# Performance work log

Hardware: AMD Instinct MI355X
Metric: run time of the kernel (lower is better)

## Reference

```python
import jax, jax.numpy as jnp
import numpy as np

TOP_K = 2


def setup_inputs() -> dict:
    key = jax.random.key(0)
    ks = jax.random.split(key, 5)
    B, S, H, E, F = 4, 1024, 1024, 16, 4096
    scale = 0.02
    return {
        "input_tensor": jax.random.normal(ks[0], (B, S, H), dtype=jnp.float32),
        "Wg": scale * jax.random.normal(ks[1], (H, E), dtype=jnp.float32),
        "bg": jnp.zeros((E,), dtype=jnp.float32),
        "W1": scale * jax.random.normal(ks[2], (E, H, F), dtype=jnp.float32),
        "b1": jnp.zeros((E, F), dtype=jnp.float32),
        "W2": scale * jax.random.normal(ks[3], (E, F, H), dtype=jnp.float32),
        "b2": jnp.zeros((E, H), dtype=jnp.float32),
    }


def reference(input_tensor, Wg, bg, W1, b1, W2, b2):
    # Faithful to DualOutputMoE.forward_first_pass: the per-(b,s,k) Python loop
    # plus _weighted_sum collapses ALL token expert outputs into a single
    # [1,1,H] vector normalized by the total routing weight (= B*S).
    B, S, H = input_tensor.shape
    T = B * S
    E = Wg.shape[1]
    x = input_tensor.reshape(T, H)

    routing_scores = x @ Wg + bg                    # [T, E] (raw gate logits)
    top_v, top_i = jax.lax.top_k(routing_scores, TOP_K)
    top_w = jax.nn.softmax(top_v, axis=-1)          # per-token top-k weights

    # combine[t, e] = sum_k top_w[t, k] * 1[top_i[t, k] == e]
    combine = jnp.zeros((T, E), x.dtype).at[jnp.arange(T)[:, None], top_i].add(top_w)
    total_weight = top_w.sum()                      # matches python sum of .item()s

    def expert_step(acc, params):
        w1, bb1, w2, bb2, c = params                # c: [T] combine weights for this expert
        y = jax.nn.gelu(x @ w1 + bb1, approximate=False) @ w2 + bb2  # [T, H]
        return acc + c @ y, None

    acc0 = jnp.zeros((H,), x.dtype)
    acc, _ = jax.lax.scan(expert_step, acc0, (W1, b1, W2, b2, combine.T))
    first_output = (acc / total_weight).reshape(1, 1, H)
    return first_output
```

## Files before the change

### kernel.cpp

```cpp
#include <hip/hip_runtime.h>
#include <hip/hip_bf16.h>
#include <math.h>

typedef __bf16 bf16_t;
typedef __bf16 bf16x4 __attribute__((ext_vector_type(4)));
typedef __bf16 bf16x8 __attribute__((ext_vector_type(8)));
typedef float  f32x4  __attribute__((ext_vector_type(4)));

#define T_TOK 4096
#define H_DIM 1024
#define E_NUM 16
#define F_DIM 4096
#define CH_ROWS 128
#define CH_MAX  32

#define WS_E0     0
#define WS_E1     16384
#define WS_W0     32768
#define WS_W1     49152
#define WS_COUNTS 65536
#define WS_SUMW   65664
#define WS_XOFF   65792
#define WS_LIDX   131072
#define WS_LW     393216
#define WS_GPART  655360
#define WS_P2     655360
#define WS_G      9043968
#define WS_XE     9306112

#define AS_GLOBAL(p) ((const __attribute__((address_space(1))) void*)(p))
#define AS_LDS(p)    ((__attribute__((address_space(3))) void*)(p))

__global__ __launch_bounds__(64) void k_route(const float* __restrict__ x,
    const float* __restrict__ Wg, const float* __restrict__ bg,
    int* __restrict__ e0, int* __restrict__ e1,
    float* __restrict__ w0, float* __restrict__ w1)
{
    const int t = blockIdx.x;
    const int lane = threadIdx.x;
    const float* xr = x + (size_t)t * H_DIM;

    float s[E_NUM];
#pragma unroll
    for (int e = 0; e < E_NUM; ++e) s[e] = 0.f;

#pragma unroll
    for (int i = 0; i < 16; ++i) {
        const int h = i * 64 + lane;
        const float xv = xr[h];
        const float4* wr = (const float4*)(Wg + (size_t)h * E_NUM);
        float4 q0 = wr[0], q1 = wr[1], q2 = wr[2], q3 = wr[3];
        s[0] += xv*q0.x;  s[1] += xv*q0.y;  s[2] += xv*q0.z;  s[3] += xv*q0.w;
        s[4] += xv*q1.x;  s[5] += xv*q1.y;  s[6] += xv*q1.z;  s[7] += xv*q1.w;
        s[8] += xv*q2.x;  s[9] += xv*q2.y;  s[10]+= xv*q2.z;  s[11]+= xv*q2.w;
        s[12]+= xv*q3.x;  s[13]+= xv*q3.y;  s[14]+= xv*q3.z;  s[15]+= xv*q3.w;
    }
#pragma unroll
    for (int off = 32; off >= 1; off >>= 1) {
#pragma unroll
        for (int e = 0; e < E_NUM; ++e) s[e] += __shfl_xor(s[e], off);
    }
    if (lane == 0) {
#pragma unroll
        for (int e = 0; e < E_NUM; ++e) s[e] += bg[e];
        float b1v = -3e38f; int i1 = 0;
#pragma unroll
        for (int e = 0; e < E_NUM; ++e) { if (s[e] > b1v) { b1v = s[e]; i1 = e; } }
        float b2v = -3e38f; int i2 = 0;
#pragma unroll
        for (int e = 0; e < E_NUM; ++e) { if (e != i1 && s[e] > b2v) { b2v = s[e]; i2 = e; } }
        const float ex  = expf(b2v - b1v);
        const float inv = 1.f / (1.f + ex);
        e0[t] = i1; e1[t] = i2;
        w0[t] = inv; w1[t] = ex * inv;
    }
}

__global__ __launch_bounds__(64) void k_lists(const int* __restrict__ e0, const int* __restrict__ e1,
    const float* __restrict__ w0, const float* __restrict__ w1,
    int* __restrict__ lidx, float* __restrict__ lw,
    int* __restrict__ counts, float* __restrict__ sumw)
{
    const int e = blockIdx.x;
    const int lane = threadIdx.x;
    int cnt = 0; float sw = 0.f;
    for (int base = 0; base < T_TOK; base += 64) {
        const int t = base + lane;
        const bool m0 = (e0[t] == e);
        const bool m1 = (e1[t] == e);
        const bool m  = m0 | m1;
        const unsigned long long bal = __ballot(m);
        const int pos = cnt + __popcll(bal & ((1ull << lane) - 1ull));
        if (m) {
            const float w = m0 ? w0[t] : w1[t];
            lidx[e * T_TOK + pos] = t;
            lw[e * T_TOK + pos]   = w;
            sw += w;
        }
        cnt += __popcll(bal);
    }
#pragma unroll
    for (int off = 32; off >= 1; off >>= 1) sw += __shfl_xor(sw, off);
    if (lane == 0) { counts[e] = cnt; sumw[e] = sw; }
}

__global__ void k_scan(const int* __restrict__ counts, int* __restrict__ xoff) {
    if (threadIdx.x == 0) {
        int o = 0;
        for (int e = 0; e < E_NUM; ++e) { xoff[e] = o; o += (counts[e] + CH_ROWS - 1) & ~(CH_ROWS - 1); }
    }
}

__global__ __launch_bounds__(256) void k_gather(const float* __restrict__ x,
    const int* __restrict__ lidx, const int* __restrict__ counts,
    const int* __restrict__ xoff, bf16_t* __restrict__ Xe)
{
    const int chunk = blockIdx.x >> 2;
    const int part  = blockIdx.x & 3;
    const int e = blockIdx.y;
    const int cnt = counts[e];
    const int start = chunk * CH_ROWS;
    if (chunk && start >= cnt) return;
    const int tid = threadIdx.x;
    const size_t rbase = (size_t)xoff[e] + start;

    for (int it = part * 16; it < part * 16 + 16; ++it) {
        const int task = it * 256 + tid;
        const int rl   = task >> 7;
        const int sc   = task & 127;
        const int row  = start + rl;
        bf16x8 v8 = {};
        if (row < cnt) {
            const int tok = lidx[e * T_TOK + row];
            const int l   = (sc & 7) ^ (rl & 7);
            const int k   = (sc >> 3) * 64 + l * 8;
            const float4 a = *(const float4*)(x + (size_t)tok * H_DIM + k);
            const float4 b = *(const float4*)(x + (size_t)tok * H_DIM + k + 4);
            v8[0]=(bf16_t)a.x; v8[1]=(bf16_t)a.y; v8[2]=(bf16_t)a.z; v8[3]=(bf16_t)a.w;
            v8[4]=(bf16_t)b.x; v8[5]=(bf16_t)b.y; v8[6]=(bf16_t)b.z; v8[7]=(bf16_t)b.w;
        }
        *(bf16x8*)(Xe + (rbase + rl) * H_DIM + sc * 8) = v8;
    }
}

__global__ __launch_bounds__(256, 3) void k_expert(
    const float* __restrict__ W1, const float* __restrict__ b1,
    const bf16_t* __restrict__ Xe, const float* __restrict__ lw,
    const int* __restrict__ counts, const int* __restrict__ xoff,
    float* __restrict__ gpart)
{
    const int ftile = blockIdx.x;
    const int chunk = blockIdx.y;
    const int e     = blockIdx.z;
    const int cnt   = counts[e];
    const int start = chunk * CH_ROWS;
    if (chunk && start >= cnt) return;

    __shared__ __align__(16) bf16_t Alds[2][CH_ROWS * 64];
    __shared__ __align__(16) bf16_t Blds[2][64 * 72];
    __shared__ float w_s[CH_ROWS];
    __shared__ float b1_s[64];
    __shared__ float gred[2][64];

    const int tid  = threadIdx.x;
    const int lane = tid & 63;
    const int wid  = tid >> 6;
    const int wm   = wid & 1;
    const int wn   = wid >> 1;
    const int lr   = lane & 15;
    const int lg   = lane >> 4;

    if (tid < CH_ROWS) {
        const int r = start + tid;
        w_s[tid] = (r < cnt) ? lw[e * T_TOK + r] : 0.f;
    } else if (tid < CH_ROWS + 64) {
        b1_s[tid - CH_ROWS] = b1[(size_t)e * F_DIM + ftile * 64 + (tid - CH_ROWS)];
    }

    f32x4 acc[4][2];
#pragma unroll
    for (int i = 0; i < 4; ++i)
#pragma unroll
        for (int j = 0; j < 2; ++j)
#pragma unroll
            for (int q = 0; q < 4; ++q) acc[i][j][q] = 0.f;

    const bf16_t* Asrc = Xe + ((size_t)xoff[e] + start) * H_DIM;
    const float*  W1p  = W1 + (size_t)e * H_DIM * F_DIM + (size_t)ftile * 64 + lane;

    const int arow = (wid * 4) * 8 + (lane >> 3);
    const int acol = lane & 7;

    float bv[16];

    {
        const float* wp = W1p + (size_t)(wid * 16) * F_DIM;
#pragma unroll
        for (int j = 0; j < 16; ++j) bv[j] = wp[(size_t)j * F_DIM];
#pragma unroll
        for (int p = 0; p < 4; ++p) {
            const int seg = wid * 4 + p;
            const bf16_t* src = Asrc + (size_t)(seg * 8 + (lane >> 3)) * H_DIM + acol * 8;
            __builtin_amdgcn_global_load_lds(AS_GLOBAL(src),
                AS_LDS((char*)&Alds[0][0] + seg * 1024), 16, 0, 0);
        }
        bf16x8 pk0, pk1;
#pragma unroll
        for (int q = 0; q < 8; ++q) { pk0[q] = (bf16_t)bv[q]; pk1[q] = (bf16_t)bv[8 + q]; }
        bf16_t* bdst = &Blds[0][lane * 72 + wid * 16];
        *(bf16x8*)bdst       = pk0;
        *(bf16x8*)(bdst + 8) = pk1;
    }
    __syncthreads();

    int cur = 0;
    for (int t = 0; t < H_DIM / 64; ++t) {
        const int nxt = cur ^ 1;
        const bool more = (t + 1) < (H_DIM / 64);
        if (more) {
            const int k0 = (t + 1) * 64;
            const float* wp = W1p + (size_t)(k0 + wid * 16) * F_DIM;
#pragma unroll
            for (int j = 0; j < 16; ++j) bv[j] = wp[(size_t)j * F_DIM];
#pragma unroll
            for (int p = 0; p < 4; ++p) {
                const int seg = wid * 4 + p;
                const bf16_t* src = Asrc + (size_t)(seg * 8 + (lane >> 3)) * H_DIM + k0 + acol * 8;
                __builtin_amdgcn_global_load_lds(AS_GLOBAL(src),
                    AS_LDS((char*)&Alds[nxt][0] + seg * 1024), 16, 0, 0);
            }
        }
#pragma unroll
        for (int kh = 0; kh < 2; ++kh) {
            bf16x8 af[4], bfr[2];
#pragma unroll
            for (int mf = 0; mf < 4; ++mf) {
                const int r = wm * 64 + mf * 16 + lr;
                const int eoff = (kh * 32 + lg * 8) ^ ((r & 7) * 8);
                af[mf] = *(const bf16x8*)&Alds[cur][r * 64 + eoff];
            }
#pragma unroll
            for (int nf = 0; nf < 2; ++nf)
                bfr[nf] = *(const bf16x8*)&Blds[cur][(wn * 32 + nf * 16 + lr) * 72 + kh * 32 + lg * 8];
#pragma unroll
            for (int mf = 0; mf < 4; ++mf)
#pragma unroll
                for (int nf = 0; nf < 2; ++nf)
                    acc[mf][nf] = __builtin_amdgcn_mfma_f32_16x16x32_bf16(af[mf], bfr[nf], acc[mf][nf], 0, 0, 0);
        }
        if (more) {
            bf16x8 pk0, pk1;
#pragma unroll
            for (int q = 0; q < 8; ++q) { pk0[q] = (bf16_t)bv[q]; pk1[q] = (bf16_t)bv[8 + q]; }
            bf16_t* bdst = &Blds[nxt][lane * 72 + wid * 16];
            *(bf16x8*)bdst       = pk0;
            *(bf16x8*)(bdst + 8) = pk1;
        }
        __syncthreads();
        cur = nxt;
    }

    float gcol[2] = {0.f, 0.f};
#pragma unroll
    for (int nf = 0; nf < 2; ++nf) {
        const float bb = b1_s[wn * 32 + nf * 16 + lr];
#pragma unroll
        for (int mf = 0; mf < 4; ++mf) {
#pragma unroll
            for (int i = 0; i < 4; ++i) {
                const int row = wm * 64 + mf * 16 + lg * 4 + i;
                const float h  = acc[mf][nf][i] + bb;
                const float gl = 0.5f * h * (1.f + erff(h * 0.70710678118654752f));
                gcol[nf] += w_s[row] * gl;
            }
        }
    }
#pragma unroll
    for (int nf = 0; nf < 2; ++nf) {
        gcol[nf] += __shfl_xor(gcol[nf], 16);
        gcol[nf] += __shfl_xor(gcol[nf], 32);
    }
    if (lane < 16) {
#pragma unroll
        for (int nf = 0; nf < 2; ++nf) gred[wm][wn * 32 + nf * 16 + lane] = gcol[nf];
    }
    __syncthreads();
    if (tid < 64) {
        const float sum = gred[0][tid] + gred[1][tid];
        gpart[(size_t)(e * CH_MAX + chunk) * F_DIM + ftile * 64 + tid] = sum;
    }
}

__global__ __launch_bounds__(256) void k_redg(const float* __restrict__ gpart,
    const int* __restrict__ counts, float* __restrict__ g)
{
    const int e = blockIdx.y;
    const int f = blockIdx.x * 256 + threadIdx.x;
    const int nch = (counts[e] + CH_ROWS - 1) / CH_ROWS;
    float s = 0.f;
    for (int c = 0; c < nch; ++c)
        s += gpart[(size_t)(e * CH_MAX + c) * F_DIM + f];
    g[(size_t)e * F_DIM + f] = s;
}

__global__ __launch_bounds__(256) void k_out1(const float* __restrict__ g,
    const float* __restrict__ W2, float* __restrict__ p2)
{
    const int fc = blockIdx.x;
    const int e  = blockIdx.y;
    const int tid = threadIdx.x;
    __shared__ float gs[128];
    if (tid < 128) gs[tid] = g[(size_t)e * F_DIM + fc * 128 + tid];
    __syncthreads();
    const float* W2p = W2 + (size_t)e * F_DIM * H_DIM + (size_t)fc * 128 * H_DIM;
    float ax = 0.f, ay = 0.f, az = 0.f, aw = 0.f;
#pragma unroll 8
    for (int f = 0; f < 128; ++f) {
        const float gv = gs[f];
        const float4 wv = *(const float4*)(W2p + (size_t)f * H_DIM + tid * 4);
        ax += gv * wv.x; ay += gv * wv.y; az += gv * wv.z; aw += gv * wv.w;
    }
    float4 st; st.x = ax; st.y = ay; st.z = az; st.w = aw;
    *(float4*)(p2 + (size_t)(e * 32 + fc) * H_DIM + tid * 4) = st;
}

__global__ __launch_bounds__(256) void k_out2(const float* __restrict__ p2,
    const float* __restrict__ sumw, const float* __restrict__ b2, float* __restrict__ out)
{
    const int tid = threadIdx.x;
    const int hh  = tid & 31;
    const int seg = tid >> 5;
    const int h   = blockIdx.x * 32 + hh;
    float s = 0.f;
    for (int j = 0; j < 64; ++j)
        s += p2[(size_t)(seg * 64 + j) * H_DIM + h];
    __shared__ float red[8][33];
    red[seg][hh] = s;
    __syncthreads();
    if (tid < 32) {
        const int h2 = blockIdx.x * 32 + tid;
        float tot = 0.f;
#pragma unroll
        for (int q = 0; q < 8; ++q) tot += red[q][tid];
        float tw = 0.f, bias = 0.f;
#pragma unroll
        for (int e = 0; e < E_NUM; ++e) { tw += sumw[e]; bias += sumw[e] * b2[e * H_DIM + h2]; }
        out[h2] = (tot + bias) / tw;
    }
}

extern "C" void kernel_launch(void* const* d_in, const int* in_sizes, int n_in,
                              void* d_out, int out_size, void* d_ws, size_t ws_size,
                              hipStream_t stream) {
    const float* x  = (const float*)d_in[0];
    const float* Wg = (const float*)d_in[1];
    const float* bg = (const float*)d_in[2];
    const float* W1 = (const float*)d_in[3];
    const float* b1 = (const float*)d_in[4];
    const float* W2 = (const float*)d_in[5];
    const float* b2 = (const float*)d_in[6];
    float* out = (float*)d_out;

    char* ws = (char*)d_ws;
    int*    e0     = (int*)(ws + WS_E0);
    int*    e1     = (int*)(ws + WS_E1);
    float*  w0     = (float*)(ws + WS_W0);
    float*  w1     = (float*)(ws + WS_W1);
    int*    counts = (int*)(ws + WS_COUNTS);
    float*  sumw   = (float*)(ws + WS_SUMW);
    int*    xoff   = (int*)(ws + WS_XOFF);
    int*    lidx   = (int*)(ws + WS_LIDX);
    float*  lw     = (float*)(ws + WS_LW);
    float*  gpart  = (float*)(ws + WS_GPART);
    float*  g      = (float*)(ws + WS_G);
    float*  p2     = (float*)(ws + WS_P2);
    bf16_t* Xe     = (bf16_t*)(ws + WS_XE);

    k_route<<<T_TOK, 64, 0, stream>>>(x, Wg, bg, e0, e1, w0, w1);
    k_lists<<<E_NUM, 64, 0, stream>>>(e0, e1, w0, w1, lidx, lw, counts, sumw);
    k_scan<<<1, 64, 0, stream>>>(counts, xoff);
    k_gather<<<dim3(CH_MAX * 4, E_NUM), 256, 0, stream>>>(x, lidx, counts, xoff, Xe);
    k_expert<<<dim3(F_DIM / 64, CH_MAX, E_NUM), 256, 0, stream>>>(W1, b1, Xe, lw, counts, xoff, gpart);
    k_redg<<<dim3(F_DIM / 256, E_NUM), 256, 0, stream>>>(gpart, counts, g);
    k_out1<<<dim3(32, E_NUM), 256, 0, stream>>>(g, W2, p2);
    k_out2<<<32, 256, 0, stream>>>(p2, sumw, b2, out);
}
```

Baseline: 313.5 us.

## Widen expert GEMM F tile to 128 and deepen W1 prefetch pipeline

Result: no change. 308.9 us (-1.5%).

```diff
diff --git a/kernel.cpp b/kernel.cpp
--- a/kernel.cpp
+++ b/kernel.cpp
@@ -143,7 +143,7 @@
     }
 }
 
-__global__ __launch_bounds__(256, 3) void k_expert(
+__global__ __launch_bounds__(256, 2) void k_expert(
     const float* __restrict__ W1, const float* __restrict__ b1,
     const bf16_t* __restrict__ Xe, const float* __restrict__ lw,
     const int* __restrict__ counts, const int* __restrict__ xoff,
@@ -157,10 +157,10 @@
     if (chunk && start >= cnt) return;
 
     __shared__ __align__(16) bf16_t Alds[2][CH_ROWS * 64];
-    __shared__ __align__(16) bf16_t Blds[2][64 * 72];
+    __shared__ __align__(16) bf16_t Blds[2][128 * 72];
     __shared__ float w_s[CH_ROWS];
-    __shared__ float b1_s[64];
-    __shared__ float gred[2][64];
+    __shared__ float b1_s[128];
+    __shared__ float gred[2][128];
 
     const int tid  = threadIdx.x;
     const int lane = tid & 63;
@@ -173,97 +173,99 @@
     if (tid < CH_ROWS) {
         const int r = start + tid;
         w_s[tid] = (r < cnt) ? lw[e * T_TOK + r] : 0.f;
-    } else if (tid < CH_ROWS + 64) {
-        b1_s[tid - CH_ROWS] = b1[(size_t)e * F_DIM + ftile * 64 + (tid - CH_ROWS)];
-    }
-
-    f32x4 acc[4][2];
+    }
+    if (tid < 128) b1_s[tid] = b1[(size_t)e * F_DIM + ftile * 128 + tid];
+
+    f32x4 acc[4][4];
 #pragma unroll
     for (int i = 0; i < 4; ++i)
 #pragma unroll
-        for (int j = 0; j < 2; ++j)
+        for (int j = 0; j < 4; ++j)
 #pragma unroll
             for (int q = 0; q < 4; ++q) acc[i][j][q] = 0.f;
 
     const bf16_t* Asrc = Xe + ((size_t)xoff[e] + start) * H_DIM;
-    const float*  W1p  = W1 + (size_t)e * H_DIM * F_DIM + (size_t)ftile * 64 + lane;
-
-    const int arow = (wid * 4) * 8 + (lane >> 3);
-    const int acol = lane & 7;
-
-    float bv[16];
-
-    {
-        const float* wp = W1p + (size_t)(wid * 16) * F_DIM;
-#pragma unroll
-        for (int j = 0; j < 16; ++j) bv[j] = wp[(size_t)j * F_DIM];
-#pragma unroll
-        for (int p = 0; p < 4; ++p) {
-            const int seg = wid * 4 + p;
-            const bf16_t* src = Asrc + (size_t)(seg * 8 + (lane >> 3)) * H_DIM + acol * 8;
-            __builtin_amdgcn_global_load_lds(AS_GLOBAL(src),
-                AS_LDS((char*)&Alds[0][0] + seg * 1024), 16, 0, 0);
-        }
-        bf16x8 pk0, pk1;
-#pragma unroll
-        for (int q = 0; q < 8; ++q) { pk0[q] = (bf16_t)bv[q]; pk1[q] = (bf16_t)bv[8 + q]; }
-        bf16_t* bdst = &Blds[0][lane * 72 + wid * 16];
-        *(bf16x8*)bdst       = pk0;
-        *(bf16x8*)(bdst + 8) = pk1;
-    }
-    __syncthreads();
-
-    int cur = 0;
-    for (int t = 0; t < H_DIM / 64; ++t) {
-        const int nxt = cur ^ 1;
-        const bool more = (t + 1) < (H_DIM / 64);
-        if (more) {
-            const int k0 = (t + 1) * 64;
-            const float* wp = W1p + (size_t)(k0 + wid * 16) * F_DIM;
-#pragma unroll
-            for (int j = 0; j < 16; ++j) bv[j] = wp[(size_t)j * F_DIM];
-#pragma unroll
-            for (int p = 0; p < 4; ++p) {
-                const int seg = wid * 4 + p;
-                const bf16_t* src = Asrc + (size_t)(seg * 8 + (lane >> 3)) * H_DIM + k0 + acol * 8;
-                __builtin_amdgcn_global_load_lds(AS_GLOBAL(src),
-                    AS_LDS((char*)&Alds[nxt][0] + seg * 1024), 16, 0, 0);
-            }
-        }
-#pragma unroll
-        for (int kh = 0; kh < 2; ++kh) {
-            bf16x8 af[4], bfr[2];
-#pragma unroll
-            for (int mf = 0; mf < 4; ++mf) {
-                const int r = wm * 64 + mf * 16 + lr;
-                const int eoff = (kh * 32 + lg * 8) ^ ((r & 7) * 8);
-                af[mf] = *(const bf16x8*)&Alds[cur][r * 64 + eoff];
-            }
-#pragma unroll
-            for (int nf = 0; nf < 2; ++nf)
-                bfr[nf] = *(const bf16x8*)&Blds[cur][(wn * 32 + nf * 16 + lr) * 72 + kh * 32 + lg * 8];
-#pragma unroll
-            for (int mf = 0; mf < 4; ++mf)
-#pragma unroll
-                for (int nf = 0; nf < 2; ++nf)
-                    acc[mf][nf] = __builtin_amdgcn_mfma_f32_16x16x32_bf16(af[mf], bfr[nf], acc[mf][nf], 0, 0, 0);
-        }
-        if (more) {
-            bf16x8 pk0, pk1;
-#pragma unroll
-            for (int q = 0; q < 8; ++q) { pk0[q] = (bf16_t)bv[q]; pk1[q] = (bf16_t)bv[8 + q]; }
-            bf16_t* bdst = &Blds[nxt][lane * 72 + wid * 16];
-            *(bf16x8*)bdst       = pk0;
-            *(bf16x8*)(bdst + 8) = pk1;
-        }
-        __syncthreads();
-        cur = nxt;
-    }
-
-    float gcol[2] = {0.f, 0.f};
-#pragma unroll
-    for (int nf = 0; nf < 2; ++nf) {
-        const float bb = b1_s[wn * 32 + nf * 16 + lr];
+    const int bf_  = tid & 127;
+    const int kh2  = tid >> 7;
+    const float* W1p = W1 + (size_t)e * H_DIM * F_DIM + (size_t)ftile * 128 + bf_;
+
+    float bvE[32], bvO[32];
+
+#define ISSUE_A(T, BUFC) { \
+    const int k0 = (T) * 64; \
+    _Pragma("unroll") \
+    for (int p = 0; p < 4; ++p) { \
+        const int seg = wid * 4 + p; \
+        const bf16_t* src = Asrc + (size_t)(seg * 8 + (lane >> 3)) * H_DIM + k0 + (lane & 7) * 8; \
+        __builtin_amdgcn_global_load_lds(AS_GLOBAL(src), \
+            AS_LDS((char*)&Alds[BUFC][0] + seg * 1024), 16, 0, 0); \
+    } }
+
+#define ISSUE_B(T, BV) { \
+    const float* wp = W1p + (size_t)((T) * 64 + kh2 * 32) * F_DIM; \
+    _Pragma("unroll") \
+    for (int j = 0; j < 32; ++j) BV[j] = wp[(size_t)j * F_DIM]; }
+
+#define WRITE_B(BUFC, BV) { \
+    _Pragma("unroll") \
+    for (int c = 0; c < 4; ++c) { \
+        bf16x8 pk; \
+        _Pragma("unroll") \
+        for (int q = 0; q < 8; ++q) pk[q] = (bf16_t)BV[c * 8 + q]; \
+        *(bf16x8*)&Blds[BUFC][bf_ * 72 + kh2 * 32 + c * 8] = pk; \
+    } }
+
+#define COMPUTE(BUFC) { \
+    _Pragma("unroll") \
+    for (int kh = 0; kh < 2; ++kh) { \
+        bf16x8 af[4], bfr[4]; \
+        _Pragma("unroll") \
+        for (int mf = 0; mf < 4; ++mf) { \
+            const int r = wm * 64 + mf * 16 + lr; \
+            const int eoff = (kh * 32 + lg * 8) ^ ((r & 7) * 8); \
+            af[mf] = *(const bf16x8*)&Alds[BUFC][r * 64 + eoff]; \
+        } \
+        _Pragma("unroll") \
+        for (int nf = 0; nf < 4; ++nf) \
+            bfr[nf] = *(const bf16x8*)&Blds[BUFC][(wn * 64 + nf * 16 + lr) * 72 + kh * 32 + lg * 8]; \
+        _Pragma("unroll") \
+        for (int mf = 0; mf < 4; ++mf) \
+            _Pragma("unroll") \
+            for (int nf = 0; nf < 4; ++nf) \
+                acc[mf][nf] = __builtin_amdgcn_mfma_f32_16x16x32_bf16(af[mf], bfr[nf], acc[mf][nf], 0, 0, 0); \
+    } }
+
+#define SB0 __builtin_amdgcn_sched_barrier(0)
+
+    ISSUE_A(0, 0); SB0;
+    ISSUE_B(0, bvE); SB0;
+    ISSUE_B(1, bvO); SB0;
+    WRITE_B(0, bvE);
+    asm volatile("s_waitcnt vmcnt(32) lgkmcnt(0)" ::: "memory");
+    SB0; __builtin_amdgcn_s_barrier(); SB0;
+
+#define KSTEP(T, CUR, NXT, BVISS, BVWR) { \
+    if ((T) < 15) { ISSUE_A((T) + 1, NXT); } SB0; \
+    if ((T) < 14) { ISSUE_B((T) + 2, BVISS); } SB0; \
+    COMPUTE(CUR); \
+    if ((T) < 15) { WRITE_B(NXT, BVWR); } \
+    if ((T) < 14) { \
+        asm volatile("s_waitcnt vmcnt(32) lgkmcnt(0)" ::: "memory"); \
+    } else { \
+        asm volatile("s_waitcnt vmcnt(0) lgkmcnt(0)" ::: "memory"); \
+    } \
+    SB0; __builtin_amdgcn_s_barrier(); SB0; }
+
+    for (int th = 0; th < 8; ++th) {
+        const int t0 = th * 2;
+        KSTEP(t0,     0, 1, bvE, bvO);
+        KSTEP(t0 + 1, 1, 0, bvO, bvE);
+    }
+
+    float gcol[4] = {0.f, 0.f, 0.f, 0.f};
+#pragma unroll
+    for (int nf = 0; nf < 4; ++nf) {
+        const float bb = b1_s[wn * 64 + nf * 16 + lr];
 #pragma unroll
         for (int mf = 0; mf < 4; ++mf) {
 #pragma unroll
@@ -276,19 +278,25 @@
         }
     }
 #pragma unroll
-    for (int nf = 0; nf < 2; ++nf) {
+    for (int nf = 0; nf < 4; ++nf) {
         gcol[nf] += __shfl_xor(gcol[nf], 16);
         gcol[nf] += __shfl_xor(gcol[nf], 32);
     }
     if (lane < 16) {
 #pragma unroll
-        for (int nf = 0; nf < 2; ++nf) gred[wm][wn * 32 + nf * 16 + lane] = gcol[nf];
+        for (int nf = 0; nf < 4; ++nf) gred[wm][wn * 64 + nf * 16 + lane] = gcol[nf];
     }
     __syncthreads();
-    if (tid < 64) {
+    if (tid < 128) {
         const float sum = gred[0][tid] + gred[1][tid];
-        gpart[(size_t)(e * CH_MAX + chunk) * F_DIM + ftile * 64 + tid] = sum;
-    }
+        gpart[(size_t)(e * CH_MAX + chunk) * F_DIM + ftile * 128 + tid] = sum;
+    }
+#undef ISSUE_A
+#undef ISSUE_B
+#undef WRITE_B
+#undef COMPUTE
+#undef KSTEP
+#undef SB0
 }
 
 __global__ __launch_bounds__(256) void k_redg(const float* __restrict__ gpart,
@@ -380,7 +388,7 @@
     k_lists<<<E_NUM, 64, 0, stream>>>(e0, e1, w0, w1, lidx, lw, counts, sumw);
     k_scan<<<1, 64, 0, stream>>>(counts, xoff);
     k_gather<<<dim3(CH_MAX * 4, E_NUM), 256, 0, stream>>>(x, lidx, counts, xoff, Xe);
-    k_expert<<<dim3(F_DIM / 64, CH_MAX, E_NUM), 256, 0, stream>>>(W1, b1, Xe, lw, counts, xoff, gpart);
+    k_expert<<<dim3(F_DIM / 128, CH_MAX, E_NUM), 256, 0, stream>>>(W1, b1, Xe, lw, counts, xoff, gpart);
     k_redg<<<dim3(F_DIM / 256, E_NUM), 256, 0, stream>>>(gpart, counts, g);
     k_out1<<<dim3(32, E_NUM), 256, 0, stream>>>(g, W2, p2);
     k_out2<<<32, 256, 0, stream>>>(p2, sumw, b2, out);
```
